# Kernel optimization log

Measured on AMD Instinct MI355X. Metric: run time of the kernel, lower is better.

Reference implementation:

```python
import jax, jax.numpy as jnp
import numpy as np

B, C, N, K = 8, 128, 4096, 16
EPS = 1e-5


def _bn(x, g, b, m, v):
    # eval-mode BatchNorm1d over channel dim of [B, C, N]
    scale = (g * jax.lax.rsqrt(v + EPS))[None, :, None]
    return x * scale + (b - m * g * jax.lax.rsqrt(v + EPS))[None, :, None]


def setup_inputs() -> dict:
    key = jax.random.key(0)
    ks = jax.random.split(key, 16)
    x = jax.random.normal(ks[0], (B, C, N), dtype=jnp.float32)
    # k incoming neighbors per node, src within the same batch graph
    src_local = jax.random.randint(ks[1], (B, N, K), 0, N)
    src = (src_local + jnp.arange(B, dtype=src_local.dtype)[:, None, None] * N).reshape(B * N, K)
    def u(k, shape, lo, hi):
        return jax.random.uniform(k, shape, jnp.float32, lo, hi)
    params = dict(
        W1=jax.random.normal(ks[2], (C, C), jnp.float32) * (1.0 / np.sqrt(C)),
        b1=jax.random.normal(ks[3], (C,), jnp.float32) * 0.02,
        g1=u(ks[4], (C,), 0.5, 1.5), be1=jax.random.normal(ks[5], (C,)) * 0.1,
        m1=jax.random.normal(ks[6], (C,)) * 0.1, v1=u(ks[7], (C,), 0.5, 1.5),
        Wmr=jax.random.normal(ks[8], (2 * C, 2 * C), jnp.float32) * (1.0 / np.sqrt(2 * C)),
        bmr=jax.random.normal(ks[9], (2 * C,), jnp.float32) * 0.02,
        W2=jax.random.normal(ks[10], (C, 2 * C), jnp.float32) * (1.0 / np.sqrt(2 * C)),
        b2=jax.random.normal(ks[11], (C,), jnp.float32) * 0.02,
        g2=u(ks[12], (C,), 0.5, 1.5), be2=jax.random.normal(ks[13], (C,)) * 0.1,
        m2=jax.random.normal(ks[14], (C,)) * 0.1, v2=u(ks[15], (C,), 0.5, 1.5),
    )
    return {"x": x, "src": src, **params}


def reference(x, src, W1, b1, g1, be1, m1, v1, Wmr, bmr, W2, b2, g2, be2, m2, v2):
    res = x
    # fc1: Conv1d(k=1) + BN, then ReLU
    h = jnp.einsum('oc,bcn->bon', W1, x) + b1[None, :, None]
    h = jax.nn.relu(_bn(h, g1, be1, m1, v1))
    # nodes: [B*N, C]
    xn = h.transpose(0, 2, 1).reshape(B * N, C)
    # MRConv: max over incoming edges of (dst - src) feature diff
    diff = xn[:, None, :] - xn[src]          # [B*N, K, C]
    max_diff = diff.max(axis=1)              # [B*N, C]
    cat = jnp.concatenate([xn, max_diff], axis=1)  # [B*N, 2C]
    hn = jax.nn.relu(cat @ Wmr.T + bmr)      # [B*N, 2C]
    h2 = hn.reshape(B, N, 2 * C).transpose(0, 2, 1)  # [B, 2C, N]
    # fc2: Conv1d(k=1) + BN
    out = jnp.einsum('oc,bcn->bon', W2, h2) + b2[None, :, None]
    out = _bn(out, g2, be2, m2, v2)
    out = out + res
    return jax.nn.relu(out)
```

## Files before the change

### kernel.cpp

```cpp
#include <hip/hip_runtime.h>


typedef short bf8_t __attribute__((ext_vector_type(8)));
typedef float f4_t  __attribute__((ext_vector_type(4)));

namespace {
constexpr int Bn = 8, Cc = 128, Nn = 4096, Kk = 16, C2 = 256;
constexpr int NODES = Bn * Nn;
constexpr float EPSf = 1e-5f;
}

__device__ __forceinline__ unsigned short f2bf(float f) {
    unsigned u = __float_as_uint(f);
    u += 0x7fffu + ((u >> 16) & 1u);
    return (unsigned short)(u >> 16);
}
__device__ __forceinline__ unsigned pk2(float a, float b) {
    return (unsigned)f2bf(a) | ((unsigned)f2bf(b) << 16);
}
__device__ __forceinline__ float bflo(unsigned u) { return __uint_as_float(u << 16); }
__device__ __forceinline__ float bfhi(unsigned u) { return __uint_as_float(u & 0xffff0000u); }
__device__ __forceinline__ unsigned diff2(unsigned o, unsigned m) {
    return pk2(bflo(o) - bflo(m), bfhi(o) - bfhi(m));
}

#define PKMIN(a, b) asm("v_pk_min_u16 %0, %0, %1" : "+v"(a) : "v"(b))

__global__ __launch_bounds__(256) void prep_kernel(
    const float* __restrict__ W1, const float* __restrict__ Wmr,
    const float* __restrict__ W2, ushort* __restrict__ W1bf,
    ushort* __restrict__ Wmrbf, ushort* __restrict__ W2bf)
{
    const int e = (blockIdx.x * 256 + threadIdx.x) * 4;
    const float* s;
    ushort* d;
    if (e < 16384)      { s = W1 + e;          d = W1bf + e; }
    else if (e < 81920) { s = Wmr + (e-16384); d = Wmrbf + (e-16384); }
    else                { s = W2 + (e-81920);  d = W2bf + (e-81920); }
    const float4 v = *(const float4*)s;
    uint2 r;
    r.x = pk2(v.x, v.y);
    r.y = pk2(v.z, v.w);
    *(uint2*)d = r;
}

__global__ __launch_bounds__(512) void fc1_mfma(
    const float* __restrict__ x, const ushort* __restrict__ W1bf,
    const float* __restrict__ b1, const float* __restrict__ g1,
    const float* __restrict__ be1, const float* __restrict__ m1,
    const float* __restrict__ v1, ushort* __restrict__ xn)
{
    __shared__ __align__(16) ushort xS[64 * 136];
    __shared__ float scS[Cc], shS[Cc];
    const int t = threadIdx.x;
    if (t < Cc) {
        const float s = g1[t] * rsqrtf(v1[t] + EPSf);
        scS[t] = s;
        shS[t] = (b1[t] - m1[t]) * s + be1[t];
    }

    const int nt0 = blockIdx.x * 64;
    const int b  = nt0 >> 12;
    const int n0 = nt0 & 4095;

    {
        const int cg = t & 31, ng = t >> 5;
        const float* xp = x + ((size_t)(b * Cc + cg * 4)) * Nn + n0 + ng * 4;
        const float4 r0 = *(const float4*)(xp + 0 * (size_t)Nn);
        const float4 r1 = *(const float4*)(xp + 1 * (size_t)Nn);
        const float4 r2 = *(const float4*)(xp + 2 * (size_t)Nn);
        const float4 r3 = *(const float4*)(xp + 3 * (size_t)Nn);
        const float c0n[4] = {r0.x, r0.y, r0.z, r0.w};
        const float c1n[4] = {r1.x, r1.y, r1.z, r1.w};
        const float c2n[4] = {r2.x, r2.y, r2.z, r2.w};
        const float c3n[4] = {r3.x, r3.y, r3.z, r3.w};
        #pragma unroll
        for (int i = 0; i < 4; ++i) {
            uint2 pk;
            pk.x = pk2(c0n[i], c1n[i]);
            pk.y = pk2(c2n[i], c3n[i]);
            *(uint2*)(xS + (ng * 4 + i) * 136 + cg * 4) = pk;
        }
    }
    __syncthreads();

    const int w = t >> 6, lane = t & 63;
    const int row16 = lane & 15, kg = lane >> 4;
    const int wr = w >> 2, wc = w & 3;

    f4_t acc[2][2];
    const f4_t zero = {0.f, 0.f, 0.f, 0.f};
    #pragma unroll
    for (int i = 0; i < 2; ++i)
        #pragma unroll
        for (int j = 0; j < 2; ++j) acc[i][j] = zero;

    #pragma unroll
    for (int ks = 0; ks < 4; ++ks) {
        const int k0 = ks * 32 + kg * 8;
        bf8_t af[2], bw[2];
        #pragma unroll
        for (int nsub = 0; nsub < 2; ++nsub)
            af[nsub] = *(const bf8_t*)(xS + (wr * 32 + nsub * 16 + row16) * 136 + k0);
        #pragma unroll
        for (int osub = 0; osub < 2; ++osub)
            bw[osub] = *(const bf8_t*)(W1bf + (wc * 32 + osub * 16 + row16) * Cc + k0);
        #pragma unroll
        for (int nsub = 0; nsub < 2; ++nsub)
            #pragma unroll
            for (int osub = 0; osub < 2; ++osub)
                acc[nsub][osub] = __builtin_amdgcn_mfma_f32_16x16x32_bf16(
                    af[nsub], bw[osub], acc[nsub][osub], 0, 0, 0);
    }

    #pragma unroll
    for (int osub = 0; osub < 2; ++osub) {
        const int o = wc * 32 + osub * 16 + row16;
        const float s = scS[o], sh = shS[o];
        #pragma unroll
        for (int nsub = 0; nsub < 2; ++nsub)
            #pragma unroll
            for (int r = 0; r < 4; ++r) {
                const int node = nt0 + wr * 32 + nsub * 16 + kg * 4 + r;
                float v = acc[nsub][osub][r] * s + sh;
                v = v > 0.f ? v : 0.f;
                xn[(size_t)node * Cc + o] = f2bf(v);
            }
    }
}

__global__ __launch_bounds__(512) void mrfc2_mfma(
    const ushort* __restrict__ xn, const int* __restrict__ src,
    const ushort* __restrict__ Wmrbf, const float* __restrict__ bmr,
    const ushort* __restrict__ W2bf, const float* __restrict__ x,
    const float* __restrict__ b2, const float* __restrict__ g2,
    const float* __restrict__ be2, const float* __restrict__ m2,
    const float* __restrict__ v2, float* __restrict__ out)
{
    __shared__ __align__(16) ushort catS[64 * 264];
    __shared__ int srcS[64 * Kk];
    __shared__ float scS[Cc], shS[Cc];
    const int t = threadIdx.x;
    const int bid = blockIdx.x;
    const int lb = (bid & 7) * 64 + (bid >> 3);
    const int node0 = lb * 64;
    const int b  = node0 >> 12;
    const int n0 = node0 & 4095;

    if (t < Cc) {
        const float s = g2[t] * rsqrtf(v2[t] + EPSf);
        scS[t] = s;
        shS[t] = (b2[t] - m2[t]) * s + be2[t];
    }
    if (t < 256)
        ((int4*)srcS)[t] = ((const int4*)(src + (size_t)node0 * Kk))[t];
    __syncthreads();

    {
        const int nl = t >> 3, q = t & 7;
        const ushort* orow = xn + (size_t)(node0 + nl) * Cc + q * 16;
        uint4 ow0 = *(const uint4*)(orow + 0);
        uint4 ow1 = *(const uint4*)(orow + 8);
        const int* sl = srcS + nl * Kk;
        const ushort* sr = xn + (size_t)sl[0] * Cc + q * 16;
        uint4 mn0 = *(const uint4*)(sr + 0);
        uint4 mn1 = *(const uint4*)(sr + 8);
        #pragma unroll
        for (int k = 1; k < Kk; ++k) {
            const ushort* s = xn + (size_t)sl[k] * Cc + q * 16;
            uint4 v0 = *(const uint4*)(s + 0);
            uint4 v1 = *(const uint4*)(s + 8);
            PKMIN(mn0.x, v0.x); PKMIN(mn0.y, v0.y); PKMIN(mn0.z, v0.z); PKMIN(mn0.w, v0.w);
            PKMIN(mn1.x, v1.x); PKMIN(mn1.y, v1.y); PKMIN(mn1.z, v1.z); PKMIN(mn1.w, v1.w);
        }
        unsigned* crow = (unsigned*)(catS + nl * 264);
        *(uint4*)(crow + q * 8 + 0) = ow0;
        *(uint4*)(crow + q * 8 + 4) = ow1;
        uint4 d0, d1;
        d0.x = diff2(ow0.x, mn0.x); d0.y = diff2(ow0.y, mn0.y);
        d0.z = diff2(ow0.z, mn0.z); d0.w = diff2(ow0.w, mn0.w);
        d1.x = diff2(ow1.x, mn1.x); d1.y = diff2(ow1.y, mn1.y);
        d1.z = diff2(ow1.z, mn1.z); d1.w = diff2(ow1.w, mn1.w);
        *(uint4*)(crow + 64 + q * 8 + 0) = d0;
        *(uint4*)(crow + 64 + q * 8 + 4) = d1;
    }
    __syncthreads();

    const int w = t >> 6, lane = t & 63;
    const int row16 = lane & 15, kg = lane >> 4;

    const int jb = w * 32;
    {
        f4_t acc[2][4];
        const f4_t zero = {0.f, 0.f, 0.f, 0.f};
        #pragma unroll
        for (int i = 0; i < 2; ++i)
            #pragma unroll
            for (int j = 0; j < 4; ++j) acc[i][j] = zero;

        #pragma unroll
        for (int ks = 0; ks < 8; ++ks) {
            const int k0 = ks * 32 + kg * 8;
            bf8_t aw[2], bc[4];
            #pragma unroll
            for (int jsub = 0; jsub < 2; ++jsub)
                aw[jsub] = *(const bf8_t*)(Wmrbf + (size_t)(jb + jsub * 16 + row16) * C2 + k0);
            #pragma unroll
            for (int nsub = 0; nsub < 4; ++nsub)
                bc[nsub] = *(const bf8_t*)(catS + (nsub * 16 + row16) * 264 + k0);
            #pragma unroll
            for (int jsub = 0; jsub < 2; ++jsub)
                #pragma unroll
                for (int nsub = 0; nsub < 4; ++nsub)
                    acc[jsub][nsub] = __builtin_amdgcn_mfma_f32_16x16x32_bf16(
                        aw[jsub], bc[nsub], acc[jsub][nsub], 0, 0, 0);
        }
        __syncthreads();

        #pragma unroll
        for (int jsub = 0; jsub < 2; ++jsub) {
            const float4 bb = *(const float4*)(bmr + jb + jsub * 16 + kg * 4);
            #pragma unroll
            for (int nsub = 0; nsub < 4; ++nsub) {
                float v0 = acc[jsub][nsub][0] + bb.x;
                float v1 = acc[jsub][nsub][1] + bb.y;
                float v2_ = acc[jsub][nsub][2] + bb.z;
                float v3 = acc[jsub][nsub][3] + bb.w;
                v0 = v0 > 0.f ? v0 : 0.f;
                v1 = v1 > 0.f ? v1 : 0.f;
                v2_ = v2_ > 0.f ? v2_ : 0.f;
                v3 = v3 > 0.f ? v3 : 0.f;
                uint2 pk;
                pk.x = pk2(v0, v1);
                pk.y = pk2(v2_, v3);
                *(uint2*)(catS + (nsub * 16 + row16) * 264 + jb + jsub * 16 + kg * 4) = pk;
            }
        }
    }
    __syncthreads();

    {
        const int ob = w * 16;
        f4_t acc[4];
        const f4_t zero = {0.f, 0.f, 0.f, 0.f};
        #pragma unroll
        for (int j = 0; j < 4; ++j) acc[j] = zero;

        #pragma unroll
        for (int ks = 0; ks < 8; ++ks) {
            const int k0 = ks * 32 + kg * 8;
            const bf8_t aw = *(const bf8_t*)(W2bf + (size_t)(ob + row16) * C2 + k0);
            #pragma unroll
            for (int nsub = 0; nsub < 4; ++nsub) {
                const bf8_t bh = *(const bf8_t*)(catS + (nsub * 16 + row16) * 264 + k0);
                acc[nsub] = __builtin_amdgcn_mfma_f32_16x16x32_bf16(aw, bh, acc[nsub], 0, 0, 0);
            }
        }

        #pragma unroll
        for (int r = 0; r < 4; ++r) {
            const int o = ob + kg * 4 + r;
            const float s = scS[o], sh = shS[o];
            const float* xr = x   + ((size_t)(b * Cc + o)) * Nn + n0;
            float*       op = out + ((size_t)(b * Cc + o)) * Nn + n0;
            #pragma unroll
            for (int nsub = 0; nsub < 4; ++nsub) {
                const int nn = nsub * 16 + row16;
                float v = acc[nsub][r] * s + sh + xr[nn];
                v = v > 0.f ? v : 0.f;
                op[nn] = v;
            }
        }
    }
}

extern "C" void kernel_launch(void* const* d_in, const int* in_sizes, int n_in,
                              void* d_out, int out_size, void* d_ws, size_t ws_size,
                              hipStream_t stream)
{
    const float* x   = (const float*)d_in[0];
    const int*   src = (const int*)  d_in[1];
    const float* W1  = (const float*)d_in[2];
    const float* b1  = (const float*)d_in[3];
    const float* g1  = (const float*)d_in[4];
    const float* be1 = (const float*)d_in[5];
    const float* m1  = (const float*)d_in[6];
    const float* v1  = (const float*)d_in[7];
    const float* Wmr = (const float*)d_in[8];
    const float* bmr = (const float*)d_in[9];
    const float* W2  = (const float*)d_in[10];
    const float* b2  = (const float*)d_in[11];
    const float* g2  = (const float*)d_in[12];
    const float* be2 = (const float*)d_in[13];
    const float* m2  = (const float*)d_in[14];
    const float* v2  = (const float*)d_in[15];
    float* out = (float*)d_out;

    ushort* W1bf  = (ushort*)d_ws;
    ushort* Wmrbf = W1bf + 16384;
    ushort* W2bf  = Wmrbf + 65536;
    ushort* xn    = W2bf + 32768;

    prep_kernel<<<112, 256, 0, stream>>>(W1, Wmr, W2, W1bf, Wmrbf, W2bf);
    fc1_mfma<<<NODES / 64, 512, 0, stream>>>(x, W1bf, b1, g1, be1, m1, v1, xn);
    mrfc2_mfma<<<NODES / 64, 512, 0, stream>>>(xn, src, Wmrbf, bmr, W2bf, x,
                                               b2, g2, be2, m2, v2, out);
}
```

Before: 42.45 us.

## Restructure fc1 MFMA tiling for vectorized bf16 stores and swizzled LDS staging

The fc1 kernel now swaps MFMA operand roles so each wave owns 16 output channels across all 64 nodes. Each lane then holds 4 consecutive channels per node and writes them as one 8-byte packed store instead of scattered 2-byte stores. The x tile is staged into LDS through an XOR swizzle with a different load pattern to cut bank conflicts. Blocks are also remapped with the same interleaved order the second kernel uses.

```diff
diff --git a/kernel.cpp b/kernel.cpp
--- a/kernel.cpp
+++ b/kernel.cpp
@@ -53,79 +53,76 @@
     __shared__ __align__(16) ushort xS[64 * 136];
     __shared__ float scS[Cc], shS[Cc];
     const int t = threadIdx.x;
+    const int bid = blockIdx.x;
+    const int lb = (bid & 7) * 64 + (bid >> 3);
+    const int node0 = lb * 64;
+    const int b  = node0 >> 12;
+    const int n0 = node0 & 4095;
+
     if (t < Cc) {
         const float s = g1[t] * rsqrtf(v1[t] + EPSf);
         scS[t] = s;
         shS[t] = (b1[t] - m1[t]) * s + be1[t];
     }
 
-    const int nt0 = blockIdx.x * 64;
-    const int b  = nt0 >> 12;
-    const int n0 = nt0 & 4095;
-
     {
-        const int cg = t & 31, ng = t >> 5;
-        const float* xp = x + ((size_t)(b * Cc + cg * 4)) * Nn + n0 + ng * 4;
-        const float4 r0 = *(const float4*)(xp + 0 * (size_t)Nn);
-        const float4 r1 = *(const float4*)(xp + 1 * (size_t)Nn);
-        const float4 r2 = *(const float4*)(xp + 2 * (size_t)Nn);
-        const float4 r3 = *(const float4*)(xp + 3 * (size_t)Nn);
-        const float c0n[4] = {r0.x, r0.y, r0.z, r0.w};
-        const float c1n[4] = {r1.x, r1.y, r1.z, r1.w};
-        const float c2n[4] = {r2.x, r2.y, r2.z, r2.w};
-        const float c3n[4] = {r3.x, r3.y, r3.z, r3.w};
-        #pragma unroll
-        for (int i = 0; i < 4; ++i) {
-            uint2 pk;
-            pk.x = pk2(c0n[i], c1n[i]);
-            pk.y = pk2(c2n[i], c3n[i]);
-            *(uint2*)(xS + (ng * 4 + i) * 136 + cg * 4) = pk;
-        }
+        const int cp = t >> 3, q = t & 7;
+        const float* p0 = x + ((size_t)(b * Cc + 2 * cp)) * Nn + n0 + q * 8;
+        const float* p1 = p0 + Nn;
+        const float4 a0 = *(const float4*)(p0);
+        const float4 a1 = *(const float4*)(p0 + 4);
+        const float4 c0 = *(const float4*)(p1);
+        const float4 c1 = *(const float4*)(p1 + 4);
+        ushort* base = xS + (size_t)q * 8 * 136 + ((cp * 2) ^ (q << 3));
+        *(unsigned*)(base + 0 * 136) = pk2(a0.x, c0.x);
+        *(unsigned*)(base + 1 * 136) = pk2(a0.y, c0.y);
+        *(unsigned*)(base + 2 * 136) = pk2(a0.z, c0.z);
+        *(unsigned*)(base + 3 * 136) = pk2(a0.w, c0.w);
+        *(unsigned*)(base + 4 * 136) = pk2(a1.x, c1.x);
+        *(unsigned*)(base + 5 * 136) = pk2(a1.y, c1.y);
+        *(unsigned*)(base + 6 * 136) = pk2(a1.z, c1.z);
+        *(unsigned*)(base + 7 * 136) = pk2(a1.w, c1.w);
     }
     __syncthreads();
 
     const int w = t >> 6, lane = t & 63;
     const int row16 = lane & 15, kg = lane >> 4;
-    const int wr = w >> 2, wc = w & 3;
-
-    f4_t acc[2][2];
+
+    f4_t acc[4];
     const f4_t zero = {0.f, 0.f, 0.f, 0.f};
     #pragma unroll
-    for (int i = 0; i < 2; ++i)
-        #pragma unroll
-        for (int j = 0; j < 2; ++j) acc[i][j] = zero;
+    for (int j = 0; j < 4; ++j) acc[j] = zero;
 
     #pragma unroll
     for (int ks = 0; ks < 4; ++ks) {
         const int k0 = ks * 32 + kg * 8;
-        bf8_t af[2], bw[2];
-        #pragma unroll
-        for (int nsub = 0; nsub < 2; ++nsub)
-            af[nsub] = *(const bf8_t*)(xS + (wr * 32 + nsub * 16 + row16) * 136 + k0);
-        #pragma unroll
-        for (int osub = 0; osub < 2; ++osub)
-            bw[osub] = *(const bf8_t*)(W1bf + (wc * 32 + osub * 16 + row16) * Cc + k0);
-        #pragma unroll
-        for (int nsub = 0; nsub < 2; ++nsub)
-            #pragma unroll
-            for (int osub = 0; osub < 2; ++osub)
-                acc[nsub][osub] = __builtin_amdgcn_mfma_f32_16x16x32_bf16(
-                    af[nsub], bw[osub], acc[nsub][osub], 0, 0, 0);
-    }
-
+        const bf8_t aw = *(const bf8_t*)(W1bf + (size_t)(w * 16 + row16) * Cc + k0);
+        #pragma unroll
+        for (int nsub = 0; nsub < 4; ++nsub) {
+            const int n = nsub * 16 + row16;
+            const bf8_t bx = *(const bf8_t*)(xS + n * 136 + (k0 ^ ((n >> 3) << 3)));
+            acc[nsub] = __builtin_amdgcn_mfma_f32_16x16x32_bf16(aw, bx, acc[nsub], 0, 0, 0);
+        }
+    }
+
+    const int o4 = w * 16 + kg * 4;
+    const float s0 = scS[o4 + 0], s1 = scS[o4 + 1], s2 = scS[o4 + 2], s3 = scS[o4 + 3];
+    const float h0 = shS[o4 + 0], h1 = shS[o4 + 1], h2 = shS[o4 + 2], h3 = shS[o4 + 3];
     #pragma unroll
-    for (int osub = 0; osub < 2; ++osub) {
-        const int o = wc * 32 + osub * 16 + row16;
-        const float s = scS[o], sh = shS[o];
-        #pragma unroll
-        for (int nsub = 0; nsub < 2; ++nsub)
-            #pragma unroll
-            for (int r = 0; r < 4; ++r) {
-                const int node = nt0 + wr * 32 + nsub * 16 + kg * 4 + r;
-                float v = acc[nsub][osub][r] * s + sh;
-                v = v > 0.f ? v : 0.f;
-                xn[(size_t)node * Cc + o] = f2bf(v);
-            }
+    for (int nsub = 0; nsub < 4; ++nsub) {
+        const int node = node0 + nsub * 16 + row16;
+        float v0 = acc[nsub][0] * s0 + h0;
+        float v1 = acc[nsub][1] * s1 + h1;
+        float v2 = acc[nsub][2] * s2 + h2;
+        float v3 = acc[nsub][3] * s3 + h3;
+        v0 = v0 > 0.f ? v0 : 0.f;
+        v1 = v1 > 0.f ? v1 : 0.f;
+        v2 = v2 > 0.f ? v2 : 0.f;
+        v3 = v3 > 0.f ? v3 : 0.f;
+        uint2 pk;
+        pk.x = pk2(v0, v1);
+        pk.y = pk2(v2, v3);
+        *(uint2*)(xn + (size_t)node * Cc + o4) = pk;
     }
 }
 
```

Result: faster. 39.51 us (-6.9%).
